# Kernel optimization log

Measured on AMD Instinct MI355X. Metric: run time of the kernel, lower is better.

The kernel has to match this reference:

```python
import jax, jax.numpy as jnp
import numpy as np

REG_MAX = 16
TOPK = 13
ALPHA = 1.0
BETA = 6.0
MATCH_W = 0.5
IOU_W = 7.5
DFL_W = 1.5
EPS = 1e-7
NEG_INF = -1e30


def _iou(b1, b2):
    # xyxy IoU, broadcastable [..., 4]
    x1 = jnp.maximum(b1[..., 0], b2[..., 0]); y1 = jnp.maximum(b1[..., 1], b2[..., 1])
    x2 = jnp.minimum(b1[..., 2], b2[..., 2]); y2 = jnp.minimum(b1[..., 3], b2[..., 3])
    inter = jnp.maximum(x2 - x1, 0.0) * jnp.maximum(y2 - y1, 0.0)
    a1 = (b1[..., 2] - b1[..., 0]) * (b1[..., 3] - b1[..., 1])
    a2 = (b2[..., 2] - b2[..., 0]) * (b2[..., 3] - b2[..., 1])
    return inter / (a1 + a2 - inter + EPS)


def _ciou(b1, b2):
    iou = _iou(b1, b2)
    w1 = b1[..., 2] - b1[..., 0]; h1 = b1[..., 3] - b1[..., 1]
    w2 = b2[..., 2] - b2[..., 0]; h2 = b2[..., 3] - b2[..., 1]
    cw = jnp.maximum(b1[..., 2], b2[..., 2]) - jnp.minimum(b1[..., 0], b2[..., 0])
    ch = jnp.maximum(b1[..., 3], b2[..., 3]) - jnp.minimum(b1[..., 1], b2[..., 1])
    c2 = cw * cw + ch * ch + EPS
    rho2 = ((b2[..., 0] + b2[..., 2] - b1[..., 0] - b1[..., 2]) ** 2
            + (b2[..., 1] + b2[..., 3] - b1[..., 1] - b1[..., 3]) ** 2) / 4.0
    v = (4.0 / jnp.pi ** 2) * (jnp.arctan(w2 / (h2 + EPS)) - jnp.arctan(w1 / (h1 + EPS))) ** 2
    a = jax.lax.stop_gradient(v / (v - iou + (1.0 + EPS)))
    return iou - (rho2 / c2 + v * a)


def _per_sample(ps, pb, bd, gtb, gtl, vcm, anchor, stride):
    # ps [N,C], pb [N,4], bd [N,4*R], gtb [M,4], gtl [M], vcm [C] bool
    N, C = ps.shape
    M = gtb.shape[0]
    lab = jnp.clip(gtl, 0, C - 1)
    gt_valid = (gtl >= 0) & (gtl < C) & vcm[lab]
    ax, ay = anchor[:, 0], anchor[:, 1]
    inside = ((ax[None, :] >= gtb[:, 0:1]) & (ax[None, :] <= gtb[:, 2:3])
              & (ay[None, :] >= gtb[:, 1:2]) & (ay[None, :] <= gtb[:, 3:4]))  # [M,N]
    iou_mn = _iou(pb[None, :, :], gtb[:, None, :])                             # [M,N]
    cls_mn = jax.nn.sigmoid(ps[:, lab]).T                                      # [M,N]
    align = jnp.where(inside & gt_valid[:, None], cls_mn ** ALPHA * iou_mn ** BETA, NEG_INF)
    top_vals, top_idx = jax.lax.top_k(align, TOPK)                             # [M,K]
    cand = jnp.full((M, N), NEG_INF, ps.dtype).at[jnp.arange(M)[:, None], top_idx].set(top_vals)
    best = cand.max(0)          # final metric per anchor
    mg = cand.argmax(0)         # winning GT (first max == earliest GT, matching loop order)
    fg = best > -1.0            # align >= 0 always; non-candidates stay at NEG_INF
    m_lab = jnp.clip(gtl[mg], 0, C - 1)
    ov = iou_mn[mg, jnp.arange(N)]
    fgf = fg.astype(ps.dtype)
    tgt_scores = jax.nn.one_hot(m_lab, C, dtype=ps.dtype) * (jnp.maximum(ov, 0.1) * fgf)[:, None]
    tb = jnp.where(fg[:, None], gtb[mg], pb)   # safe target boxes (masked out when not fg)

    # classification BCE over valid classes (mean)
    bce = jnp.maximum(ps, 0.0) - ps * tgt_scores + jnp.log1p(jnp.exp(-jnp.abs(ps)))
    vc = vcm.astype(ps.dtype)
    match = (bce * vc[None, :]).sum() / (N * jnp.maximum(vc.sum(), 1.0))

    cnt = fg.sum()
    ciou_v = _ciou(pb, tb)
    iou_loss = jnp.where(cnt > 0, ((1.0 - ciou_v) * fgf).sum() / jnp.maximum(cnt, 1), 0.0)
    miou_sum = (_iou(pb, tb) * fgf).sum()
    probs = jax.nn.sigmoid(ps)
    pos_sum = (probs[jnp.arange(N), m_lab] * fgf).sum()

    # DFL
    d = jnp.concatenate([anchor - tb[:, :2], tb[:, 2:] - anchor], -1) / stride  # [N,4]
    d = jnp.clip(d, 0.0, REG_MAX - 1 - 0.01)
    tl = d.astype(jnp.int32)
    tr = jnp.minimum(tl + 1, REG_MAX - 1)
    wl = tr.astype(ps.dtype) - d
    wr = 1.0 - wl
    logp = jax.nn.log_softmax(bd.reshape(N, 4, REG_MAX), -1)
    ll = -jnp.take_along_axis(logp, tl[..., None], -1)[..., 0]
    lr = -jnp.take_along_axis(logp, tr[..., None], -1)[..., 0]
    dfl = jnp.where(cnt > 0, ((ll * wl + lr * wr) * fgf[:, None]).sum() / jnp.maximum(cnt * 4, 1), 0.0)

    mx = jnp.where(vcm[None, :], probs, NEG_INF).max(-1)
    neg_sum = (mx * (1.0 - fgf)).sum()
    neg_cnt = N - cnt
    return match, iou_loss, dfl, cnt, neg_cnt, pos_sum, neg_sum, miou_sum


def setup_inputs() -> dict:
    key = jax.random.key(0)
    B, N, C, M, R = 16, 8400, 80, 64, REG_MAX
    ks = jax.random.split(key, 7)
    pts, sts = [], []
    for s in (8, 16, 32):
        n = 640 // s
        g = (np.arange(n) + 0.5) * s
        xv, yv = np.meshgrid(g, g)
        pts.append(np.stack([xv.ravel(), yv.ravel()], 1))
        sts.append(np.full((n * n, 1), s, np.float32))
    anchor_points = jnp.asarray(np.concatenate(pts).astype(np.float32))  # [8400,2]
    stride_tensor = jnp.asarray(np.concatenate(sts))                      # [8400,1]
    c = anchor_points[None] + jax.random.normal(ks[0], (B, N, 2)) * stride_tensor[None]
    wh = jax.random.uniform(ks[1], (B, N, 2), minval=8.0, maxval=128.0)
    pred_boxes = jnp.concatenate([jnp.clip(c - wh / 2, 0.0, 640.0),
                                  jnp.clip(c + wh / 2, 0.0, 640.0)], -1)
    gc = jax.random.uniform(ks[2], (B, M, 2), minval=64.0, maxval=576.0)
    gwh = jax.random.uniform(ks[3], (B, M, 2), minval=16.0, maxval=128.0)
    gt_boxes = jnp.concatenate([gc - gwh / 2, gc + gwh / 2], -1)
    gt_labels = jax.random.randint(ks[4], (B, M), 0, C)
    class_mask = jnp.ones((B, C), bool)
    pred_scores = jax.random.normal(ks[5], (B, N, C))
    box_distribution = jax.random.normal(ks[6], (B, N, 4 * R))
    return {"pred_scores": pred_scores, "pred_boxes": pred_boxes,
            "anchor_points": anchor_points, "stride_tensor": stride_tensor,
            "box_distribution": box_distribution, "gt_boxes": gt_boxes,
            "gt_labels": gt_labels, "class_mask": class_mask}


def reference(pred_scores, pred_boxes, anchor_points, stride_tensor,
              box_distribution, gt_boxes, gt_labels, class_mask):
    B = pred_scores.shape[0]
    f = lambda ps, pb, bd, gtb, gtl, vcm: _per_sample(ps, pb, bd, gtb, gtl, vcm,
                                                      anchor_points, stride_tensor)
    match, iou_l, dfl, cnt, ncnt, psum, nsum, misum = jax.vmap(f)(
        pred_scores, pred_boxes, box_distribution, gt_boxes, gt_labels, class_mask)
    tot_pos = cnt.sum()
    tot_neg = ncnt.sum()
    total_match = match.sum(); total_iou = iou_l.sum(); total_dfl = dfl.sum()
    loss = (MATCH_W * total_match + IOU_W * total_iou + DFL_W * total_dfl) / B
    mean_pos = psum.sum() / jnp.maximum(tot_pos, 1)
    mean_neg = nsum.sum() / jnp.maximum(tot_neg, 1)
    mean_miou = misum.sum() / jnp.maximum(tot_pos, 1)
    return (loss, total_match / B, total_iou / B, total_dfl / B,
            tot_pos.astype(jnp.float32), mean_pos, mean_neg, mean_miou)
```

## Files before the change

kernel.cpp:

```cpp
#include <hip/hip_runtime.h>
#include <stdint.h>

#define TOPK 13
#define NEG_INF_F (-1e30f)
#define EPSF 1e-7f
#define L2EF 1.4426950408889634f
#define LN2F 0.6931471805599453f
#define MAXCAND 2048

__device__ __forceinline__ int mask_at(const uint8_t* __restrict__ raw, int i) {
    bool as_u8 = (raw[1] | raw[2] | raw[3]) != 0;
    return as_u8 ? (raw[i] != 0) : (((const int*)raw)[i] != 0);
}

__device__ __forceinline__ float iou_pair(float ax1, float ay1, float ax2, float ay2,
                                          float bx1, float by1, float bx2, float by2) {
    float x1 = fmaxf(ax1, bx1), y1 = fmaxf(ay1, by1);
    float x2 = fminf(ax2, bx2), y2 = fminf(ay2, by2);
    float inter = fmaxf(x2 - x1, 0.f) * fmaxf(y2 - y1, 0.f);
    float a1 = (ax2 - ax1) * (ay2 - ay1);
    float a2 = (bx2 - bx1) * (by2 - by1);
    return inter / (a1 + a2 - inter + EPSF);
}

__device__ __forceinline__ float sigmoid_fast(float s) {
    return 1.f / (1.f + exp2f(-s * L2EF));
}
__device__ __forceinline__ float softplus_bce(float s) {
    float t = exp2f(-fabsf(s) * L2EF);
    return fmaxf(s, 0.f) + log2f(1.f + t) * LN2F;
}

__global__ __launch_bounds__(256) void assign_topk_k(
    const float* __restrict__ ps, const float* __restrict__ pb,
    const float* __restrict__ anch, const float* __restrict__ gtb,
    const int* __restrict__ gtl, const uint8_t* __restrict__ mraw,
    unsigned long long* __restrict__ best, int B, int N, int C, int M) {
    int b = blockIdx.x % B;
    int m = blockIdx.x / B;

    __shared__ float cval[MAXCAND];
    __shared__ int   cidx[MAXCAND];
    __shared__ int   scnt;
    if (threadIdx.x == 0) scnt = 0;

    int lbl = gtl[b * M + m];
    int lab = min(max(lbl, 0), C - 1);
    bool valid = (lbl >= 0) && (lbl < C) && (mask_at(mraw, b * C + lab) != 0);
    __syncthreads();

    if (valid) {
        float4 g = ((const float4*)gtb)[(size_t)b * M + m];
        const float* psb = ps + (size_t)b * N * C + lab;
        const float4* pbb = (const float4*)pb + (size_t)b * N;
        for (int n = threadIdx.x; n < N; n += 256) {
            float2 a = ((const float2*)anch)[n];
            if (a.x < g.x || a.x > g.z || a.y < g.y || a.y > g.w) continue;
            float4 p = pbb[n];
            float iou = iou_pair(p.x, p.y, p.z, p.w, g.x, g.y, g.z, g.w);
            float s = psb[(size_t)n * C];
            float sig = sigmoid_fast(s);
            float i3 = iou * iou * iou;
            float val = sig * i3 * i3;
            int slot = atomicAdd(&scnt, 1);
            if (slot < MAXCAND) { cval[slot] = val; cidx[slot] = n; }
        }
    }
    __syncthreads();
    if (!valid || threadIdx.x >= 64) return;

    int total = min(scnt, MAXCAND);
    if (total == 0) return;
    int lane = threadIdx.x;

    float lv[TOPK];
    int   li[TOPK];
#pragma unroll
    for (int j = 0; j < TOPK; ++j) { lv[j] = NEG_INF_F; li[j] = -1; }
    for (int i = lane; i < total; i += 64) {
        float v = cval[i]; int ix = cidx[i];
        if (v > lv[TOPK - 1]) {
            bool placed = false;
#pragma unroll
            for (int j = TOPK - 1; j >= 1; --j) {
                if (!placed) {
                    if (v > lv[j - 1]) { lv[j] = lv[j - 1]; li[j] = li[j - 1]; }
                    else { lv[j] = v; li[j] = ix; placed = true; }
                }
            }
            if (!placed) { lv[0] = v; li[0] = ix; }
        }
    }

    unsigned key = 0xFFFFFFFFu - (unsigned)m;
    unsigned long long* bb = best + (size_t)b * N;
    int rounds = min(total, TOPK);
    for (int p = 0; p < rounds; ++p) {
        float bv = lv[0]; int bl = lane;
        for (int off = 32; off > 0; off >>= 1) {
            float ov = __shfl_down(bv, off, 64);
            int   ol = __shfl_down(bl, off, 64);
            if (ov > bv) { bv = ov; bl = ol; }
        }
        bl = __shfl(bl, 0, 64);
        if (lane == bl) {
            unsigned long long pk =
                ((unsigned long long)__float_as_uint(lv[0]) << 32) | (unsigned long long)key;
            atomicMax(bb + li[0], pk);
#pragma unroll
            for (int j = 0; j < TOPK - 1; ++j) { lv[j] = lv[j + 1]; li[j] = li[j + 1]; }
            lv[TOPK - 1] = NEG_INF_F; li[TOPK - 1] = -1;
        }
    }
}

__global__ __launch_bounds__(256) void per_anchor_k(
    const float* __restrict__ ps, const float* __restrict__ pb,
    const float* __restrict__ anch, const float* __restrict__ strd,
    const float* __restrict__ bd, const float* __restrict__ gtb,
    const int* __restrict__ gtl, const uint8_t* __restrict__ mraw,
    const unsigned long long* __restrict__ best,
    float* __restrict__ partials, int B, int N, int C, int M) {
    int b = blockIdx.y;
    int n = blockIdx.x * 256 + threadIdx.x;

    __shared__ int smask[256];
    __shared__ int s_all;
    __shared__ float sred[4 * 8];
    if (threadIdx.x == 0) s_all = 1;
    __syncthreads();
    for (int c = threadIdx.x; c < C && c < 256; c += 256) {
        int v = mask_at(mraw, b * C + c);
        smask[c] = v;
        if (!v) atomicExch(&s_all, 0);
    }
    __syncthreads();
    bool allm = (s_all != 0);

    float acc0 = 0, acc1 = 0, acc2 = 0, acc3 = 0, acc4 = 0, acc5 = 0, acc6 = 0;

    if (n < N) {
        unsigned long long pk = best[(size_t)b * N + n];
        bool fg = (pk != 0ull);
        int mg = fg ? (int)(0xFFFFFFFFu - (unsigned)(pk & 0xFFFFFFFFull)) : 0;
        int lbl = gtl[b * M + mg];
        int m_lab = min(max(lbl, 0), C - 1);

        const float* psr = ps + ((size_t)b * N + n) * C;
        float bce_sum = 0.f, smax = NEG_INF_F;
        int c4 = C & ~3;
        if (allm) {
            for (int c = 0; c < c4; c += 4) {
                float4 s4 = *(const float4*)(psr + c);
                bce_sum += softplus_bce(s4.x) + softplus_bce(s4.y) +
                           softplus_bce(s4.z) + softplus_bce(s4.w);
                smax = fmaxf(smax, fmaxf(fmaxf(s4.x, s4.y), fmaxf(s4.z, s4.w)));
            }
            for (int c = c4; c < C; ++c) {
                float s = psr[c];
                bce_sum += softplus_bce(s);
                smax = fmaxf(smax, s);
            }
        } else {
            for (int c = 0; c < C; ++c) {
                float s = psr[c];
                if (smask[c]) { bce_sum += softplus_bce(s); smax = fmaxf(smax, s); }
            }
        }

        float fgf = fg ? 1.f : 0.f;
        acc1 = fgf;
        acc3 = fg ? 0.f : sigmoid_fast(smax);

        if (fg) {
            float slab = psr[m_lab];
            float4 p = ((const float4*)pb)[(size_t)b * N + n];
            float4 g = ((const float4*)gtb)[(size_t)b * M + mg];
            float ov = iou_pair(p.x, p.y, p.z, p.w, g.x, g.y, g.z, g.w);
            bce_sum -= fmaxf(ov, 0.1f) * slab;
            acc2 = sigmoid_fast(slab);
            acc4 = ov;
            float w1 = p.z - p.x, h1 = p.w - p.y;
            float w2 = g.z - g.x, h2 = g.w - g.y;
            float cw = fmaxf(p.z, g.z) - fminf(p.x, g.x);
            float ch = fmaxf(p.w, g.w) - fminf(p.y, g.y);
            float c2 = cw * cw + ch * ch + EPSF;
            float dx = g.x + g.z - p.x - p.z;
            float dy = g.y + g.w - p.y - p.w;
            float rho2 = (dx * dx + dy * dy) * 0.25f;
            const float PI = 3.14159265358979323846f;
            float dv = atanf(w2 / (h2 + EPSF)) - atanf(w1 / (h1 + EPSF));
            float v = (4.f / (PI * PI)) * dv * dv;
            float a = v / (v - ov + 1.f + EPSF);
            acc5 = 1.f - (ov - (rho2 / c2 + v * a));
            float2 an = ((const float2*)anch)[n];
            float stv = strd[n];
            float dvals[4] = { (an.x - g.x) / stv, (an.y - g.y) / stv,
                               (g.z - an.x) / stv, (g.w - an.y) / stv };
            const float* bdr = bd + ((size_t)b * N + n) * 64;
            float dfl = 0.f;
            for (int k = 0; k < 4; ++k) {
                float xs[16];
                float mxv = NEG_INF_F;
#pragma unroll
                for (int j = 0; j < 16; ++j) { xs[j] = bdr[k * 16 + j]; mxv = fmaxf(mxv, xs[j]); }
                float se = 0.f;
#pragma unroll
                for (int j = 0; j < 16; ++j) se += exp2f((xs[j] - mxv) * L2EF);
                float lse = mxv + log2f(se) * LN2F;
                float d = fminf(fmaxf(dvals[k], 0.f), 14.99f);
                int tl = (int)d;
                int tr = min(tl + 1, 15);
                float wl = (float)tr - d;
                float wr = 1.f - wl;
                float xtl = bdr[k * 16 + tl];
                float xtr = bdr[k * 16 + tr];
                dfl += (lse - xtl) * wl + (lse - xtr) * wr;
            }
            acc6 = dfl;
        }
        acc0 = bce_sum;
    }

    int lane = threadIdx.x & 63, wid = threadIdx.x >> 6;
    float accs[7] = { acc0, acc1, acc2, acc3, acc4, acc5, acc6 };
#pragma unroll
    for (int j = 0; j < 7; ++j) {
        float v = accs[j];
        for (int off = 32; off > 0; off >>= 1) v += __shfl_down(v, off, 64);
        if (lane == 0) sred[wid * 8 + j] = v;
    }
    __syncthreads();
    if (threadIdx.x < 7) {
        float s = sred[0 * 8 + threadIdx.x] + sred[1 * 8 + threadIdx.x] +
                  sred[2 * 8 + threadIdx.x] + sred[3 * 8 + threadIdx.x];
        atomicAdd(&partials[b * 8 + threadIdx.x], s);
    }
}

__global__ void finalize_k(const float* __restrict__ partials, const uint8_t* __restrict__ mraw,
                           float* __restrict__ out, int B, int N, int C) {
    int lane = threadIdx.x;
    float tm = 0, ti = 0, td = 0, tp = 0, tneg = 0, pos = 0, neg = 0, miou = 0;
    if (lane < B) {
        float vcs = 0.f;
        for (int c = 0; c < C; ++c) vcs += mask_at(mraw, lane * C + c) ? 1.f : 0.f;
        const float* pr = partials + lane * 8;
        float cnt = pr[1];
        tm = pr[0] / ((float)N * fmaxf(vcs, 1.f));
        ti = (cnt > 0.f) ? pr[5] / fmaxf(cnt, 1.f) : 0.f;
        td = (cnt > 0.f) ? pr[6] / fmaxf(cnt * 4.f, 1.f) : 0.f;
        tp = cnt; tneg = (float)N - cnt;
        pos = pr[2]; neg = pr[3]; miou = pr[4];
    }
    for (int off = 32; off > 0; off >>= 1) {
        tm += __shfl_down(tm, off, 64);   ti += __shfl_down(ti, off, 64);
        td += __shfl_down(td, off, 64);   tp += __shfl_down(tp, off, 64);
        tneg += __shfl_down(tneg, off, 64); pos += __shfl_down(pos, off, 64);
        neg += __shfl_down(neg, off, 64); miou += __shfl_down(miou, off, 64);
    }
    if (lane == 0) {
        float Bf = (float)B;
        out[0] = (0.5f * tm + 7.5f * ti + 1.5f * td) / Bf;
        out[1] = tm / Bf;
        out[2] = ti / Bf;
        out[3] = td / Bf;
        out[4] = tp;
        out[5] = pos / fmaxf(tp, 1.f);
        out[6] = neg / fmaxf(tneg, 1.f);
        out[7] = miou / fmaxf(tp, 1.f);
    }
}

extern "C" void kernel_launch(void* const* d_in, const int* in_sizes, int n_in,
                              void* d_out, int out_size, void* d_ws, size_t ws_size,
                              hipStream_t stream) {
    const float* ps   = (const float*)d_in[0];
    const float* pb   = (const float*)d_in[1];
    const float* anch = (const float*)d_in[2];
    const float* strd = (const float*)d_in[3];
    const float* bd   = (const float*)d_in[4];
    const float* gtb  = (const float*)d_in[5];
    const int*   gtl  = (const int*)d_in[6];
    const uint8_t* cmsk = (const uint8_t*)d_in[7];

    int N = in_sizes[2] / 2;
    int B = in_sizes[1] / (4 * N);
    int C = in_sizes[0] / (B * N);
    int M = in_sizes[6] / B;

    unsigned long long* best = (unsigned long long*)d_ws;
    size_t off = (size_t)B * N * sizeof(unsigned long long);
    off = (off + 255) & ~(size_t)255;
    float* partials = (float*)((char*)d_ws + off);
    size_t total = off + (size_t)B * 8 * sizeof(float);

    hipMemsetAsync(d_ws, 0, total, stream);
    assign_topk_k<<<B * M, 256, 0, stream>>>(ps, pb, anch, gtb, gtl, cmsk, best, B, N, C, M);
    dim3 gB((N + 255) / 256, B);
    per_anchor_k<<<gB, 256, 0, stream>>>(ps, pb, anch, strd, bd, gtb, gtl, cmsk, best,
                                         partials, B, N, C, M);
    finalize_k<<<1, 64, 0, stream>>>(partials, cmsk, (float*)d_out, B, N, C);
}
```

Before: 175.6 us.

## Split each anchor across two lanes and fold finalize into last block

The per-anchor kernel now assigns two threads per anchor, each handling half the class scores and half the DFL sides, combined with a lane-pair shuffle. Twice as many blocks are launched. The separate finalize kernel is removed: a global atomic counter lets the last block to finish compute the final outputs. This aims to raise parallelism and memory-level concurrency on the per-anchor pass and save one kernel launch, at the cost of an extra shuffle and a serialized tail in the last block.

```diff
diff --git a/kernel.cpp b/kernel.cpp
--- a/kernel.cpp
+++ b/kernel.cpp
@@ -120,22 +120,26 @@
     const float* __restrict__ bd, const float* __restrict__ gtb,
     const int* __restrict__ gtl, const uint8_t* __restrict__ mraw,
     const unsigned long long* __restrict__ best,
-    float* __restrict__ partials, int B, int N, int C, int M) {
+    float* __restrict__ partials, int* __restrict__ done_ctr,
+    float* __restrict__ out, int B, int N, int C, int M) {
     int b = blockIdx.y;
-    int n = blockIdx.x * 256 + threadIdx.x;
+    int half = threadIdx.x & 1;
+    int n = blockIdx.x * 128 + (threadIdx.x >> 1);
 
     __shared__ int smask[256];
-    __shared__ int s_all;
+    __shared__ int s_notall;
     __shared__ float sred[4 * 8];
-    if (threadIdx.x == 0) s_all = 1;
+    __shared__ int s_last;
+    if (threadIdx.x == 0) s_notall = 0;
     __syncthreads();
     for (int c = threadIdx.x; c < C && c < 256; c += 256) {
         int v = mask_at(mraw, b * C + c);
         smask[c] = v;
-        if (!v) atomicExch(&s_all, 0);
-    }
-    __syncthreads();
-    bool allm = (s_all != 0);
+        if (!v) s_notall = 1;
+    }
+    __syncthreads();
+    bool allm = (s_notall == 0);
+    bool pairable = ((C & 7) == 0);
 
     float acc0 = 0, acc1 = 0, acc2 = 0, acc3 = 0, acc4 = 0, acc5 = 0, acc6 = 0;
 
@@ -148,58 +152,46 @@
 
         const float* psr = ps + ((size_t)b * N + n) * C;
         float bce_sum = 0.f, smax = NEG_INF_F;
-        int c4 = C & ~3;
-        if (allm) {
-            for (int c = 0; c < c4; c += 4) {
-                float4 s4 = *(const float4*)(psr + c);
-                bce_sum += softplus_bce(s4.x) + softplus_bce(s4.y) +
-                           softplus_bce(s4.z) + softplus_bce(s4.w);
-                smax = fmaxf(smax, fmaxf(fmaxf(s4.x, s4.y), fmaxf(s4.z, s4.w)));
-            }
-            for (int c = c4; c < C; ++c) {
-                float s = psr[c];
-                bce_sum += softplus_bce(s);
-                smax = fmaxf(smax, s);
-            }
-        } else {
+
+        if (pairable) {
+            int h4 = C >> 3;
+            const float4* p4 = (const float4*)psr + half * h4;
+            if (allm) {
+                for (int i = 0; i < h4; ++i) {
+                    float4 s4 = p4[i];
+                    bce_sum += softplus_bce(s4.x) + softplus_bce(s4.y) +
+                               softplus_bce(s4.z) + softplus_bce(s4.w);
+                    smax = fmaxf(smax, fmaxf(fmaxf(s4.x, s4.y), fmaxf(s4.z, s4.w)));
+                }
+            } else {
+                int cbase = half * (C >> 1);
+                for (int c = 0; c < (C >> 1); ++c) {
+                    float s = psr[cbase + c];
+                    if (smask[cbase + c]) { bce_sum += softplus_bce(s); smax = fmaxf(smax, s); }
+                }
+            }
+            bce_sum += __shfl_xor(bce_sum, 1, 64);
+            smax = fmaxf(smax, __shfl_xor(smax, 1, 64));
+        } else if (half == 0) {
             for (int c = 0; c < C; ++c) {
                 float s = psr[c];
-                if (smask[c]) { bce_sum += softplus_bce(s); smax = fmaxf(smax, s); }
-            }
-        }
-
-        float fgf = fg ? 1.f : 0.f;
-        acc1 = fgf;
-        acc3 = fg ? 0.f : sigmoid_fast(smax);
+                if (allm || smask[c]) { bce_sum += softplus_bce(s); smax = fmaxf(smax, s); }
+            }
+        }
 
         if (fg) {
-            float slab = psr[m_lab];
             float4 p = ((const float4*)pb)[(size_t)b * N + n];
             float4 g = ((const float4*)gtb)[(size_t)b * M + mg];
             float ov = iou_pair(p.x, p.y, p.z, p.w, g.x, g.y, g.z, g.w);
-            bce_sum -= fmaxf(ov, 0.1f) * slab;
-            acc2 = sigmoid_fast(slab);
-            acc4 = ov;
-            float w1 = p.z - p.x, h1 = p.w - p.y;
-            float w2 = g.z - g.x, h2 = g.w - g.y;
-            float cw = fmaxf(p.z, g.z) - fminf(p.x, g.x);
-            float ch = fmaxf(p.w, g.w) - fminf(p.y, g.y);
-            float c2 = cw * cw + ch * ch + EPSF;
-            float dx = g.x + g.z - p.x - p.z;
-            float dy = g.y + g.w - p.y - p.w;
-            float rho2 = (dx * dx + dy * dy) * 0.25f;
-            const float PI = 3.14159265358979323846f;
-            float dv = atanf(w2 / (h2 + EPSF)) - atanf(w1 / (h1 + EPSF));
-            float v = (4.f / (PI * PI)) * dv * dv;
-            float a = v / (v - ov + 1.f + EPSF);
-            acc5 = 1.f - (ov - (rho2 / c2 + v * a));
             float2 an = ((const float2*)anch)[n];
             float stv = strd[n];
-            float dvals[4] = { (an.x - g.x) / stv, (an.y - g.y) / stv,
-                               (g.z - an.x) / stv, (g.w - an.y) / stv };
+            float dall[4] = { (an.x - g.x) / stv, (an.y - g.y) / stv,
+                              (g.z - an.x) / stv, (g.w - an.y) / stv };
             const float* bdr = bd + ((size_t)b * N + n) * 64;
+            int k0 = pairable ? half * 2 : 0;
+            int k1 = pairable ? half * 2 + 2 : 4;
             float dfl = 0.f;
-            for (int k = 0; k < 4; ++k) {
+            for (int k = k0; k < k1; ++k) {
                 float xs[16];
                 float mxv = NEG_INF_F;
 #pragma unroll
@@ -208,18 +200,41 @@
 #pragma unroll
                 for (int j = 0; j < 16; ++j) se += exp2f((xs[j] - mxv) * L2EF);
                 float lse = mxv + log2f(se) * LN2F;
-                float d = fminf(fmaxf(dvals[k], 0.f), 14.99f);
+                float d = fminf(fmaxf(dall[k], 0.f), 14.99f);
                 int tl = (int)d;
                 int tr = min(tl + 1, 15);
                 float wl = (float)tr - d;
-                float wr = 1.f - wl;
                 float xtl = bdr[k * 16 + tl];
                 float xtr = bdr[k * 16 + tr];
-                dfl += (lse - xtl) * wl + (lse - xtr) * wr;
-            }
-            acc6 = dfl;
-        }
-        acc0 = bce_sum;
+                dfl += (lse - xtl) * wl + (lse - xtr) * (1.f - wl);
+            }
+            if (pairable) dfl += __shfl_xor(dfl, 1, 64);
+
+            if (half == 0 || !pairable) {
+                float slab = psr[m_lab];
+                bce_sum -= fmaxf(ov, 0.1f) * slab;
+                acc1 = 1.f;
+                acc2 = sigmoid_fast(slab);
+                acc4 = ov;
+                float w1 = p.z - p.x, h1 = p.w - p.y;
+                float w2 = g.z - g.x, h2 = g.w - g.y;
+                float cw = fmaxf(p.z, g.z) - fminf(p.x, g.x);
+                float ch = fmaxf(p.w, g.w) - fminf(p.y, g.y);
+                float c2 = cw * cw + ch * ch + EPSF;
+                float dx = g.x + g.z - p.x - p.z;
+                float dy = g.y + g.w - p.y - p.w;
+                float rho2 = (dx * dx + dy * dy) * 0.25f;
+                const float PI = 3.14159265358979323846f;
+                float dv = atanf(w2 / (h2 + EPSF)) - atanf(w1 / (h1 + EPSF));
+                float v = (4.f / (PI * PI)) * dv * dv;
+                float a = v / (v - ov + 1.f + EPSF);
+                acc5 = 1.f - (ov - (rho2 / c2 + v * a));
+                acc6 = dfl;
+            }
+        } else if (half == 0 || !pairable) {
+            acc3 = sigmoid_fast(smax);
+        }
+        if (half == 0 || !pairable) acc0 = bce_sum;
     }
 
     int lane = threadIdx.x & 63, wid = threadIdx.x >> 6;
@@ -236,39 +251,47 @@
                   sred[2 * 8 + threadIdx.x] + sred[3 * 8 + threadIdx.x];
         atomicAdd(&partials[b * 8 + threadIdx.x], s);
     }
-}
-
-__global__ void finalize_k(const float* __restrict__ partials, const uint8_t* __restrict__ mraw,
-                           float* __restrict__ out, int B, int N, int C) {
-    int lane = threadIdx.x;
-    float tm = 0, ti = 0, td = 0, tp = 0, tneg = 0, pos = 0, neg = 0, miou = 0;
-    if (lane < B) {
-        float vcs = 0.f;
-        for (int c = 0; c < C; ++c) vcs += mask_at(mraw, lane * C + c) ? 1.f : 0.f;
-        const float* pr = partials + lane * 8;
-        float cnt = pr[1];
-        tm = pr[0] / ((float)N * fmaxf(vcs, 1.f));
-        ti = (cnt > 0.f) ? pr[5] / fmaxf(cnt, 1.f) : 0.f;
-        td = (cnt > 0.f) ? pr[6] / fmaxf(cnt * 4.f, 1.f) : 0.f;
-        tp = cnt; tneg = (float)N - cnt;
-        pos = pr[2]; neg = pr[3]; miou = pr[4];
-    }
-    for (int off = 32; off > 0; off >>= 1) {
-        tm += __shfl_down(tm, off, 64);   ti += __shfl_down(ti, off, 64);
-        td += __shfl_down(td, off, 64);   tp += __shfl_down(tp, off, 64);
-        tneg += __shfl_down(tneg, off, 64); pos += __shfl_down(pos, off, 64);
-        neg += __shfl_down(neg, off, 64); miou += __shfl_down(miou, off, 64);
-    }
-    if (lane == 0) {
-        float Bf = (float)B;
-        out[0] = (0.5f * tm + 7.5f * ti + 1.5f * td) / Bf;
-        out[1] = tm / Bf;
-        out[2] = ti / Bf;
-        out[3] = td / Bf;
-        out[4] = tp;
-        out[5] = pos / fmaxf(tp, 1.f);
-        out[6] = neg / fmaxf(tneg, 1.f);
-        out[7] = miou / fmaxf(tp, 1.f);
+    __syncthreads();
+    if (threadIdx.x == 0) {
+        int prev = __hip_atomic_fetch_add(done_ctr, 1, __ATOMIC_ACQ_REL,
+                                          __HIP_MEMORY_SCOPE_AGENT);
+        s_last = (prev == (int)(gridDim.x * gridDim.y) - 1) ? 1 : 0;
+    }
+    __syncthreads();
+    if (s_last && threadIdx.x < 64) {
+        int l = threadIdx.x;
+        float tm = 0, ti = 0, td = 0, tp = 0, tneg = 0, pos = 0, neg = 0, miou = 0;
+        if (l < B) {
+            float vcs = 0.f;
+            for (int c = 0; c < C; ++c) vcs += mask_at(mraw, l * C + c) ? 1.f : 0.f;
+            float pr[7];
+            for (int j = 0; j < 7; ++j)
+                pr[j] = __hip_atomic_load(&partials[l * 8 + j], __ATOMIC_ACQUIRE,
+                                          __HIP_MEMORY_SCOPE_AGENT);
+            float cnt = pr[1];
+            tm = pr[0] / ((float)N * fmaxf(vcs, 1.f));
+            ti = (cnt > 0.f) ? pr[5] / fmaxf(cnt, 1.f) : 0.f;
+            td = (cnt > 0.f) ? pr[6] / fmaxf(cnt * 4.f, 1.f) : 0.f;
+            tp = cnt; tneg = (float)N - cnt;
+            pos = pr[2]; neg = pr[3]; miou = pr[4];
+        }
+        for (int off = 32; off > 0; off >>= 1) {
+            tm += __shfl_down(tm, off, 64);     ti += __shfl_down(ti, off, 64);
+            td += __shfl_down(td, off, 64);     tp += __shfl_down(tp, off, 64);
+            tneg += __shfl_down(tneg, off, 64); pos += __shfl_down(pos, off, 64);
+            neg += __shfl_down(neg, off, 64);   miou += __shfl_down(miou, off, 64);
+        }
+        if (l == 0) {
+            float Bf = (float)B;
+            out[0] = (0.5f * tm + 7.5f * ti + 1.5f * td) / Bf;
+            out[1] = tm / Bf;
+            out[2] = ti / Bf;
+            out[3] = td / Bf;
+            out[4] = tp;
+            out[5] = pos / fmaxf(tp, 1.f);
+            out[6] = neg / fmaxf(tneg, 1.f);
+            out[7] = miou / fmaxf(tp, 1.f);
+        }
     }
 }
 
@@ -293,12 +316,14 @@
     size_t off = (size_t)B * N * sizeof(unsigned long long);
     off = (off + 255) & ~(size_t)255;
     float* partials = (float*)((char*)d_ws + off);
-    size_t total = off + (size_t)B * 8 * sizeof(float);
+    size_t off2 = off + (size_t)B * 8 * sizeof(float);
+    off2 = (off2 + 255) & ~(size_t)255;
+    int* done_ctr = (int*)((char*)d_ws + off2);
+    size_t total = off2 + 256;
 
     hipMemsetAsync(d_ws, 0, total, stream);
     assign_topk_k<<<B * M, 256, 0, stream>>>(ps, pb, anch, gtb, gtl, cmsk, best, B, N, C, M);
-    dim3 gB((N + 255) / 256, B);
+    dim3 gB((N + 127) / 128, B);
     per_anchor_k<<<gB, 256, 0, stream>>>(ps, pb, anch, strd, bd, gtb, gtl, cmsk, best,
-                                         partials, B, N, C, M);
-    finalize_k<<<1, 64, 0, stream>>>(partials, cmsk, (float*)d_out, B, N, C);
-}
+                                         partials, done_ctr, (float*)d_out, B, N, C, M);
+}
```

Result: slower. 196.3 us (+11.8%).
